# Optimization experiments

Measured on AMD Instinct MI355X. Metric: run time of the kernel, lower is better.

## Reference

```python
import jax, jax.numpy as jnp
import numpy as np

EPS = 1e-5

def _bn_relu(x, g, b, m, v):
    # inference batchnorm + relu, NCHW, fused affine
    scale = g * jax.lax.rsqrt(v + EPS)
    shift = b - m * scale
    return jnp.maximum(x * scale[None, :, None, None] + shift[None, :, None, None], 0.0)

def _conv1x1(x, w):
    # x: [B,C,H,W], w: [O,C]
    return jnp.einsum('bchw,oc->bohw', x, w)

def _xcorr_depthwise(search, kernel, padding=0):
    # search: [B,C,Hs,Ws], kernel: [B,C,Hk,Wk]; grouped conv, groups=B*C
    B, C, Hs, Ws = search.shape
    Hk, Wk = kernel.shape[2], kernel.shape[3]
    x = search.reshape(1, B * C, Hs, Ws)
    k = kernel.reshape(B * C, 1, Hk, Wk)
    out = jax.lax.conv_general_dilated(
        x, k, window_strides=(1, 1), padding=[(padding, padding), (padding, padding)],
        feature_group_count=B * C, dimension_numbers=('NCHW', 'OIHW', 'NCHW'))
    return out.reshape(B, C, out.shape[2], out.shape[3])

def setup_inputs():
    key = jax.random.key(0)
    ks = jax.random.split(key, 20)
    B, Cin, HID, COUT = 128, 256, 256, 20
    s = 1.0 / np.sqrt(Cin)
    inp = {
        'kernel': jax.random.normal(ks[0], (B, Cin, 7, 7), jnp.float32),
        'search': jax.random.normal(ks[1], (B, Cin, 31, 31), jnp.float32),
        # conv_kernel branch (1x1 conv weight stored as [O,C]) + BN stats
        'w_k': jax.random.normal(ks[2], (HID, Cin), jnp.float32) * s,
        'g_k': 1.0 + 0.1 * jax.random.normal(ks[3], (HID,), jnp.float32),
        'b_k': 0.1 * jax.random.normal(ks[4], (HID,), jnp.float32),
        'm_k': 0.1 * jax.random.normal(ks[5], (HID,), jnp.float32),
        'v_k': jax.random.uniform(ks[6], (HID,), jnp.float32, 0.5, 1.5),
        # conv_search branch
        'w_s': jax.random.normal(ks[7], (HID, Cin), jnp.float32) * s,
        'g_s': 1.0 + 0.1 * jax.random.normal(ks[8], (HID,), jnp.float32),
        'b_s': 0.1 * jax.random.normal(ks[9], (HID,), jnp.float32),
        'm_s': 0.1 * jax.random.normal(ks[10], (HID,), jnp.float32),
        'v_s': jax.random.uniform(ks[11], (HID,), jnp.float32, 0.5, 1.5),
        # head: conv1(1x1)+BN+ReLU, conv2(1x1, bias)
        'w_h1': jax.random.normal(ks[12], (HID, HID), jnp.float32) * (1.0 / np.sqrt(HID)),
        'g_h': 1.0 + 0.1 * jax.random.normal(ks[13], (HID,), jnp.float32),
        'b_h': 0.1 * jax.random.normal(ks[14], (HID,), jnp.float32),
        'm_h': 0.1 * jax.random.normal(ks[15], (HID,), jnp.float32),
        'v_h': jax.random.uniform(ks[16], (HID,), jnp.float32, 0.5, 1.5),
        'w_h2': jax.random.normal(ks[17], (COUT, HID), jnp.float32) * (1.0 / np.sqrt(HID)),
        'bias_h2': 0.1 * jax.random.normal(ks[18], (COUT,), jnp.float32),
    }
    return inp

def reference(kernel, search, w_k, g_k, b_k, m_k, v_k, w_s, g_s, b_s, m_s, v_s,
              w_h1, g_h, b_h, m_h, v_h, w_h2, bias_h2):
    k = _bn_relu(_conv1x1(kernel, w_k), g_k, b_k, m_k, v_k)   # [B,256,7,7]
    s = _bn_relu(_conv1x1(search, w_s), g_s, b_s, m_s, v_s)   # [B,256,31,31]
    feat = _xcorr_depthwise(s, k, padding=0)                  # [B,256,25,25]
    y = _bn_relu(_conv1x1(feat, w_h1), g_h, b_h, m_h, v_h)
    out = _conv1x1(y, w_h2) + bias_h2[None, :, None, None]    # [B,20,25,25]
    return out
```

## Files before the change

### kernel.cpp

```cpp
#include <hip/hip_runtime.h>
#include <hip/hip_fp16.h>

typedef _Float16 f16;
typedef __attribute__((ext_vector_type(8))) _Float16 f16x8;
typedef __attribute__((ext_vector_type(4))) _Float16 f16x4;
typedef __attribute__((ext_vector_type(2))) _Float16 f16x2;
typedef __attribute__((ext_vector_type(4))) float f32x4;

#define MFMA16(a, b, c) __builtin_amdgcn_mfma_f32_16x16x32_f16((a), (b), (c), 0, 0, 0)

#define OFF_WK   0u
#define OFF_WS   131072u
#define OFF_WH1  262144u
#define OFF_W2P  393216u
#define OFF_SH   409600u
#define OFF_S    412672u
#define OFF_KF   63392768u
#define OFF_FEAT 66604032u

__global__ __launch_bounds__(256) void prep_weights(
    const float* __restrict__ wk, const float* __restrict__ gk, const float* __restrict__ bk,
    const float* __restrict__ mk, const float* __restrict__ vk,
    const float* __restrict__ wsr, const float* __restrict__ gs, const float* __restrict__ bs,
    const float* __restrict__ ms, const float* __restrict__ vs,
    const float* __restrict__ wh1, const float* __restrict__ gh, const float* __restrict__ bh,
    const float* __restrict__ mh, const float* __restrict__ vh,
    const float* __restrict__ wh2,
    f16* __restrict__ wk16, f16* __restrict__ ws16, f16* __restrict__ wh116,
    f16* __restrict__ w2p, float* __restrict__ shifts) {
  int o = blockIdx.x;
  int t = threadIdx.x;
  float sck = gk[o] * rsqrtf(vk[o] + 1e-5f);
  float scs = gs[o] * rsqrtf(vs[o] + 1e-5f);
  float sch = gh[o] * rsqrtf(vh[o] + 1e-5f);
  int idx = o * 256 + t;
  wk16[idx]  = (f16)(wk[idx] * sck);
  ws16[idx]  = (f16)(wsr[idx] * scs);
  wh116[idx] = (f16)(wh1[idx] * sch);
  if (o < 32) w2p[idx] = (o < 20) ? (f16)wh2[idx] : (f16)0;
  if (t == 0) {
    shifts[o]       = bk[o] - mk[o] * sck;
    shifts[256 + o] = bs[o] - ms[o] * scs;
    shifts[512 + o] = bh[o] - mh[o] * sch;
  }
}

__device__ __forceinline__ int pi_row(int q, int r) {
  return (q ^ (r << 2)) + (r << 4);
}

template <int P>
__global__ __launch_bounds__(256) void conv_nchw(
    const float* __restrict__ X, const f16* __restrict__ W,
    const float* __restrict__ shift, f16* __restrict__ out) {
  const int C = 256;
  int n0 = blockIdx.x * 64;
  int t = threadIdx.x;
  int lane = t & 63, wave = t >> 6;
  int fm = lane & 15, kg = lane >> 4;

  __shared__ f16 Bs[2][64 * 40];

  int b0 = n0 / P, bp0 = n0 - b0 * P;
  bool safe = (bp0 + 64 <= P);

  int px = (t & 15) * 4;
  int cpr = (t >> 4) * 2;
  const float* xb = X + ((size_t)b0 * C) * P + bp0 + px;

  int ub[4], up[4];
  if (!safe) {
#pragma unroll
    for (int e = 0; e < 4; ++e) {
      int gn = n0 + px + e;
      ub[e] = gn / P;
      up[e] = gn - ub[e] * P;
    }
  }

  int wrow[4];
#pragma unroll
  for (int e = 0; e < 4; ++e) wrow[e] = pi_row(t & 15, e);
  int rrow[4];
#pragma unroll
  for (int nf = 0; nf < 4; ++nf) rrow[nf] = pi_row(nf * 4 + (fm >> 2), fm & 3);

  const f16* wp = W + (size_t)(wave * 64 + fm) * C + kg * 8;

  f32x4 rb[3][2];
#pragma unroll
  for (int s = 0; s < 3; ++s) {
    int cl = s * 32 + cpr;
    if (safe) {
      rb[s][0] = *(const f32x4*)(xb + (size_t)cl * P);
      rb[s][1] = *(const f32x4*)(xb + (size_t)(cl + 1) * P);
    } else {
#pragma unroll
      for (int e = 0; e < 4; ++e) {
        rb[s][0][e] = X[((size_t)ub[e] * C + cl) * P + up[e]];
        rb[s][1][e] = X[((size_t)ub[e] * C + cl + 1) * P + up[e]];
      }
    }
  }

  f32x4 acc[4][4] = {};
#pragma unroll
  for (int ci = 0; ci < 8; ++ci) {
    f16x8 a[4];
#pragma unroll
    for (int of = 0; of < 4; ++of)
      a[of] = *(const f16x8*)(wp + (size_t)of * 16 * C + ci * 32);

    f16* buf = Bs[ci & 1];
#pragma unroll
    for (int e = 0; e < 4; ++e) {
      f16x2 v;
      v[0] = (f16)rb[ci % 3][0][e];
      v[1] = (f16)rb[ci % 3][1][e];
      *(f16x2*)&buf[wrow[e] * 40 + cpr] = v;
    }
    if (ci + 3 < 8) {
      int cl = (ci + 3) * 32 + cpr;
      if (safe) {
        rb[ci % 3][0] = *(const f32x4*)(xb + (size_t)cl * P);
        rb[ci % 3][1] = *(const f32x4*)(xb + (size_t)(cl + 1) * P);
      } else {
#pragma unroll
        for (int e = 0; e < 4; ++e) {
          rb[ci % 3][0][e] = X[((size_t)ub[e] * C + cl) * P + up[e]];
          rb[ci % 3][1][e] = X[((size_t)ub[e] * C + cl + 1) * P + up[e]];
        }
      }
    }
    asm volatile("s_waitcnt lgkmcnt(0)" ::: "memory");
    __builtin_amdgcn_s_barrier();

    f16x8 b[4];
#pragma unroll
    for (int nf = 0; nf < 4; ++nf)
      b[nf] = *(const f16x8*)&buf[rrow[nf] * 40 + kg * 8];
#pragma unroll
    for (int of = 0; of < 4; ++of)
#pragma unroll
      for (int nf = 0; nf < 4; ++nf)
        acc[of][nf] = MFMA16(a[of], b[nf], acc[of][nf]);
  }

#pragma unroll
  for (int of = 0; of < 4; ++of) {
    int orow = wave * 64 + of * 16 + kg * 4;
    f32x4 sh = *(const f32x4*)(shift + orow);
#pragma unroll
    for (int nf = 0; nf < 4; ++nf) {
      int n = n0 + nf * 16 + fm;
      f16x4 st;
#pragma unroll
      for (int r = 0; r < 4; ++r)
        st[r] = (f16)fmaxf(acc[of][nf][r] + sh[r], 0.0f);
      *(f16x4*)(out + (size_t)n * C + orow) = st;
    }
  }
}

__global__ __launch_bounds__(256) void xcorr_dw_row(
    const f16* __restrict__ S ,
    const f16* __restrict__ K ,
    f16* __restrict__ F ) {
  int id = blockIdx.x;
  int x = id & 7;
  int r = id >> 3;
  int g = r % 7;
  int bq = r / 7;
  int b = bq * 8 + x;

  int wave = threadIdx.x >> 6;
  int lane = threadIdx.x & 63;
  int oi = g * 4 + wave;
  if (oi >= 25) return;

  const f16* Sb = S + (size_t)b * 961 * 256 + lane * 4;
  const f16* Kb = K + (size_t)b * 49 * 256 + lane * 4;

  f16x4 acc[25] = {};

  for (int di = 0; di < 7; ++di) {
    const f16* sp = Sb + (size_t)(oi + di) * 31 * 256;
    f16x4 srow[31];
#pragma unroll
    for (int j = 0; j < 31; ++j) srow[j] = *(const f16x4*)(sp + (size_t)j * 256);
    const f16* kp = Kb + (size_t)di * 7 * 256;
    f16x4 krow[7];
#pragma unroll
    for (int j = 0; j < 7; ++j) krow[j] = *(const f16x4*)(kp + (size_t)j * 256);

#pragma unroll
    for (int dj = 0; dj < 7; ++dj) {
      f16x4 kv = krow[dj];
#pragma unroll
      for (int oj = 0; oj < 25; ++oj)
        acc[oj] += srow[oj + dj] * kv;
    }
  }

  f16* Fb = F + ((size_t)b * 625 + (size_t)oi * 25) * 256 + lane * 4;
#pragma unroll
  for (int oj = 0; oj < 25; ++oj)
    *(f16x4*)(Fb + (size_t)oj * 256) = acc[oj];
}

__global__ __launch_bounds__(256) void head_fused(
    const f16* __restrict__ Xt ,
    const f16* __restrict__ W1, const float* __restrict__ shift,
    const f16* __restrict__ W2p , const float* __restrict__ bias,
    float* __restrict__ out ) {
  const int C = 256;
  int n0 = blockIdx.x * 64;
  int t = threadIdx.x;
  int lane = t & 63, wave = t >> 6;
  int fm = lane & 15, kg = lane >> 4;

  __shared__ f16 Ys[32][64][8];

  const f16* wp = W1 + (size_t)(wave * 64 + fm) * C + kg * 8;
  const f16* xp = Xt + (size_t)(n0 + fm) * C + kg * 8;

  f32x4 acc[4][4] = {};
#pragma unroll
  for (int c0 = 0; c0 < 256; c0 += 32) {
    f16x8 a[4], b[4];
#pragma unroll
    for (int of = 0; of < 4; ++of) a[of] = *(const f16x8*)(wp + (size_t)of * 16 * C + c0);
#pragma unroll
    for (int nf = 0; nf < 4; ++nf) b[nf] = *(const f16x8*)(xp + (size_t)nf * 16 * C + c0);
#pragma unroll
    for (int of = 0; of < 4; ++of)
#pragma unroll
      for (int nf = 0; nf < 4; ++nf)
        acc[of][nf] = MFMA16(a[of], b[nf], acc[of][nf]);
  }

#pragma unroll
  for (int of = 0; of < 4; ++of) {
    int orow = wave * 64 + of * 16 + kg * 4;
#pragma unroll
    for (int nf = 0; nf < 4; ++nf) {
      int n = nf * 16 + fm;
      f16x4 st;
#pragma unroll
      for (int r = 0; r < 4; ++r)
        st[r] = (f16)fmaxf(acc[of][nf][r] + shift[orow + r], 0.0f);
      *(f16x4*)&Ys[orow >> 3][n][(kg & 1) * 4] = st;
    }
  }
  __syncthreads();

  f32x4 acc2[2] = {};
#pragma unroll
  for (int c0 = 0; c0 < 256; c0 += 32) {
    f16x8 b = *(const f16x8*)&Ys[(c0 >> 3) + kg][wave * 16 + fm][0];
    f16x8 a0 = *(const f16x8*)(W2p + (size_t)fm * C + c0 + kg * 8);
    f16x8 a1 = *(const f16x8*)(W2p + (size_t)(16 + fm) * C + c0 + kg * 8);
    acc2[0] = MFMA16(a0, b, acc2[0]);
    acc2[1] = MFMA16(a1, b, acc2[1]);
  }

  int n = n0 + wave * 16 + fm;
  int bq = n / 625, bp = n - bq * 625;
  float* op = out + (size_t)bq * 12500 + bp;
#pragma unroll
  for (int of = 0; of < 2; ++of) {
#pragma unroll
    for (int r = 0; r < 4; ++r) {
      int o = of * 16 + kg * 4 + r;
      if (o < 20) op[(size_t)o * 625] = acc2[of][r] + bias[o];
    }
  }
}

extern "C" void kernel_launch(void* const* d_in, const int* in_sizes, int n_in,
                              void* d_out, int out_size, void* d_ws, size_t ws_size,
                              hipStream_t stream) {
  const float* kernel_in = (const float*)d_in[0];
  const float* search    = (const float*)d_in[1];
  const float* w_k = (const float*)d_in[2];
  const float* g_k = (const float*)d_in[3];
  const float* b_k = (const float*)d_in[4];
  const float* m_k = (const float*)d_in[5];
  const float* v_k = (const float*)d_in[6];
  const float* w_s = (const float*)d_in[7];
  const float* g_s = (const float*)d_in[8];
  const float* b_s = (const float*)d_in[9];
  const float* m_s = (const float*)d_in[10];
  const float* v_s = (const float*)d_in[11];
  const float* w_h1 = (const float*)d_in[12];
  const float* g_h = (const float*)d_in[13];
  const float* b_h = (const float*)d_in[14];
  const float* m_h = (const float*)d_in[15];
  const float* v_h = (const float*)d_in[16];
  const float* w_h2 = (const float*)d_in[17];
  const float* bias_h2 = (const float*)d_in[18];
  float* out = (float*)d_out;

  char* ws = (char*)d_ws;
  f16* wk16  = (f16*)(ws + OFF_WK);
  f16* ws16  = (f16*)(ws + OFF_WS);
  f16* wh116 = (f16*)(ws + OFF_WH1);
  f16* w2p   = (f16*)(ws + OFF_W2P);
  float* shifts = (float*)(ws + OFF_SH);
  f16* sbuf = (f16*)(ws + OFF_S);
  f16* kbuf = (f16*)(ws + OFF_KF);
  f16* fbuf = (f16*)(ws + OFF_FEAT);

  prep_weights<<<256, 256, 0, stream>>>(w_k, g_k, b_k, m_k, v_k,
                                        w_s, g_s, b_s, m_s, v_s,
                                        w_h1, g_h, b_h, m_h, v_h, w_h2,
                                        wk16, ws16, wh116, w2p, shifts);

  conv_nchw<961><<<dim3(1922), 256, 0, stream>>>(search, ws16, shifts + 256, sbuf);
  conv_nchw<49><<<dim3(98), 256, 0, stream>>>(kernel_in, wk16, shifts + 0, kbuf);

  xcorr_dw_row<<<dim3(896), 256, 0, stream>>>(sbuf, kbuf, fbuf);

  head_fused<<<dim3(1250), 256, 0, stream>>>(
      fbuf, wh116, shifts + 512, w2p, bias_h2, out);
}
```

Before: 172.5 us.

## Fuse depthwise xcorr with head convolutions via shared-memory feature tile

Merges the depthwise cross-correlation kernel and the two-layer 1x1 head into a single kernel. Each block computes up to 4 output rows (100 positions, padded to 112) of the xcorr result into an XOR-swizzled LDS tile, then runs both head GEMMs with MFMA directly from LDS. This removes the round trip of the 128x625x256 f16 feature map through global memory and one kernel launch. In exchange it uses 56KB of LDS per block, which may lower occupancy, wastes MFMA work on padded rows, and only reaches 896 blocks for the head stage.

```diff
diff --git a/kernel.cpp b/kernel.cpp
--- a/kernel.cpp
+++ b/kernel.cpp
@@ -16,7 +16,6 @@
 #define OFF_SH   409600u
 #define OFF_S    412672u
 #define OFF_KF   63392768u
-#define OFF_FEAT 66604032u
 
 __global__ __launch_bounds__(256) void prep_weights(
     const float* __restrict__ wk, const float* __restrict__ gk, const float* __restrict__ bk,
@@ -162,117 +161,136 @@
   }
 }
 
-__global__ __launch_bounds__(256) void xcorr_dw_row(
+__global__ __launch_bounds__(256) void xcorr_head(
     const f16* __restrict__ S ,
-    const f16* __restrict__ K ,
-    f16* __restrict__ F ) {
+    const f16* __restrict__ Kf ,
+    const f16* __restrict__ W1, const float* __restrict__ shift,
+    const f16* __restrict__ W2p, const float* __restrict__ bias,
+    float* __restrict__ out ) {
+  const int C = 256;
   int id = blockIdx.x;
   int x = id & 7;
   int r = id >> 3;
   int g = r % 7;
-  int bq = r / 7;
-  int b = bq * 8 + x;
-
-  int wave = threadIdx.x >> 6;
-  int lane = threadIdx.x & 63;
-  int oi = g * 4 + wave;
-  if (oi >= 25) return;
-
-  const f16* Sb = S + (size_t)b * 961 * 256 + lane * 4;
-  const f16* Kb = K + (size_t)b * 49 * 256 + lane * 4;
-
-  f16x4 acc[25] = {};
-
-  for (int di = 0; di < 7; ++di) {
-    const f16* sp = Sb + (size_t)(oi + di) * 31 * 256;
-    f16x4 srow[31];
-#pragma unroll
-    for (int j = 0; j < 31; ++j) srow[j] = *(const f16x4*)(sp + (size_t)j * 256);
-    const f16* kp = Kb + (size_t)di * 7 * 256;
-    f16x4 krow[7];
-#pragma unroll
-    for (int j = 0; j < 7; ++j) krow[j] = *(const f16x4*)(kp + (size_t)j * 256);
-
-#pragma unroll
-    for (int dj = 0; dj < 7; ++dj) {
-      f16x4 kv = krow[dj];
-#pragma unroll
-      for (int oj = 0; oj < 25; ++oj)
-        acc[oj] += srow[oj + dj] * kv;
-    }
-  }
-
-  f16* Fb = F + ((size_t)b * 625 + (size_t)oi * 25) * 256 + lane * 4;
-#pragma unroll
-  for (int oj = 0; oj < 25; ++oj)
-    *(f16x4*)(Fb + (size_t)oj * 256) = acc[oj];
-}
-
-__global__ __launch_bounds__(256) void head_fused(
-    const f16* __restrict__ Xt ,
-    const f16* __restrict__ W1, const float* __restrict__ shift,
-    const f16* __restrict__ W2p , const float* __restrict__ bias,
-    float* __restrict__ out ) {
-  const int C = 256;
-  int n0 = blockIdx.x * 64;
+  int b = (r / 7) * 8 + x;
+
   int t = threadIdx.x;
-  int lane = t & 63, wave = t >> 6;
+  int w = t >> 6, lane = t & 63;
   int fm = lane & 15, kg = lane >> 4;
-
-  __shared__ f16 Ys[32][64][8];
-
-  const f16* wp = W1 + (size_t)(wave * 64 + fm) * C + kg * 8;
-  const f16* xp = Xt + (size_t)(n0 + fm) * C + kg * 8;
-
-  f32x4 acc[4][4] = {};
-#pragma unroll
-  for (int c0 = 0; c0 < 256; c0 += 32) {
-    f16x8 a[4], b[4];
-#pragma unroll
-    for (int of = 0; of < 4; ++of) a[of] = *(const f16x8*)(wp + (size_t)of * 16 * C + c0);
-#pragma unroll
-    for (int nf = 0; nf < 4; ++nf) b[nf] = *(const f16x8*)(xp + (size_t)nf * 16 * C + c0);
+  int oi = g * 4 + w;
+
+  __shared__ char F[112 * 512];
+
+  if (oi < 25) {
+    const f16* Sb = S + (size_t)b * 961 * 256 + lane * 4;
+    const f16* Kb = Kf + (size_t)b * 49 * 256 + lane * 4;
+    f16x4 acc[25] = {};
+    for (int di = 0; di < 7; ++di) {
+      const f16* sp = Sb + (size_t)(oi + di) * 31 * 256;
+      f16x4 srow[31];
+#pragma unroll
+      for (int j = 0; j < 31; ++j) srow[j] = *(const f16x4*)(sp + (size_t)j * 256);
+      const f16* kp = Kb + (size_t)di * 7 * 256;
+      f16x4 krow[7];
+#pragma unroll
+      for (int j = 0; j < 7; ++j) krow[j] = *(const f16x4*)(kp + (size_t)j * 256);
+#pragma unroll
+      for (int dj = 0; dj < 7; ++dj) {
+        f16x4 kv = krow[dj];
+#pragma unroll
+        for (int oj = 0; oj < 25; ++oj)
+          acc[oj] += srow[oj + dj] * kv;
+      }
+    }
+#pragma unroll
+    for (int oj = 0; oj < 25; ++oj) {
+      int n = w * 25 + oj;
+      *(f16x4*)(F + ((n * 512 + lane * 8) ^ ((n & 7) << 4))) = acc[oj];
+    }
+  } else {
+    f16x4 z = {};
+#pragma unroll
+    for (int oj = 0; oj < 25; ++oj) {
+      int n = w * 25 + oj;
+      *(f16x4*)(F + ((n * 512 + lane * 8) ^ ((n & 7) << 4))) = z;
+    }
+  }
+  __syncthreads();
+
+  const f16* wp = W1 + (size_t)(w * 64 + fm) * C + kg * 8;
+  f32x4 acc1[4][7] = {};
+#pragma unroll
+  for (int ci = 0; ci < 8; ++ci) {
+    f16x8 a[4];
 #pragma unroll
     for (int of = 0; of < 4; ++of)
-#pragma unroll
-      for (int nf = 0; nf < 4; ++nf)
-        acc[of][nf] = MFMA16(a[of], b[nf], acc[of][nf]);
-  }
+      a[of] = *(const f16x8*)(wp + (size_t)of * 16 * C + ci * 32);
+    f16x8 bf[7];
+#pragma unroll
+    for (int nf = 0; nf < 7; ++nf) {
+      int n = nf * 16 + fm;
+      bf[nf] = *(const f16x8*)(F + ((n * 512 + (ci * 32 + kg * 8) * 2) ^ ((n & 7) << 4)));
+    }
+#pragma unroll
+    for (int of = 0; of < 4; ++of)
+#pragma unroll
+      for (int nf = 0; nf < 7; ++nf)
+        acc1[of][nf] = MFMA16(a[of], bf[nf], acc1[of][nf]);
+  }
+  __syncthreads();
 
 #pragma unroll
   for (int of = 0; of < 4; ++of) {
-    int orow = wave * 64 + of * 16 + kg * 4;
-#pragma unroll
-    for (int nf = 0; nf < 4; ++nf) {
+    int orow = w * 64 + of * 16 + kg * 4;
+    f32x4 sh = *(const f32x4*)(shift + orow);
+#pragma unroll
+    for (int nf = 0; nf < 7; ++nf) {
       int n = nf * 16 + fm;
       f16x4 st;
 #pragma unroll
-      for (int r = 0; r < 4; ++r)
-        st[r] = (f16)fmaxf(acc[of][nf][r] + shift[orow + r], 0.0f);
-      *(f16x4*)&Ys[orow >> 3][n][(kg & 1) * 4] = st;
+      for (int q = 0; q < 4; ++q)
+        st[q] = (f16)fmaxf(acc1[of][nf][q] + sh[q], 0.0f);
+      *(f16x4*)(F + ((n * 512 + orow * 2) ^ ((n & 7) << 4))) = st;
     }
   }
   __syncthreads();
 
-  f32x4 acc2[2] = {};
-#pragma unroll
-  for (int c0 = 0; c0 < 256; c0 += 32) {
-    f16x8 b = *(const f16x8*)&Ys[(c0 >> 3) + kg][wave * 16 + fm][0];
-    f16x8 a0 = *(const f16x8*)(W2p + (size_t)fm * C + c0 + kg * 8);
-    f16x8 a1 = *(const f16x8*)(W2p + (size_t)(16 + fm) * C + c0 + kg * 8);
-    acc2[0] = MFMA16(a0, b, acc2[0]);
-    acc2[1] = MFMA16(a1, b, acc2[1]);
-  }
-
-  int n = n0 + wave * 16 + fm;
-  int bq = n / 625, bp = n - bq * 625;
-  float* op = out + (size_t)bq * 12500 + bp;
-#pragma unroll
-  for (int of = 0; of < 2; ++of) {
-#pragma unroll
-    for (int r = 0; r < 4; ++r) {
-      int o = of * 16 + kg * 4 + r;
-      if (o < 20) op[(size_t)o * 625] = acc2[of][r] + bias[o];
+  f32x4 acc2[2][2] = {};
+  int nfa = w, nfb = w + 4;
+#pragma unroll
+  for (int ci = 0; ci < 8; ++ci) {
+    f16x8 a0 = *(const f16x8*)(W2p + (size_t)fm * C + ci * 32 + kg * 8);
+    f16x8 a1 = *(const f16x8*)(W2p + (size_t)(16 + fm) * C + ci * 32 + kg * 8);
+    int na = nfa * 16 + fm;
+    f16x8 b0 = *(const f16x8*)(F + ((na * 512 + (ci * 32 + kg * 8) * 2) ^ ((na & 7) << 4)));
+    acc2[0][0] = MFMA16(a0, b0, acc2[0][0]);
+    acc2[1][0] = MFMA16(a1, b0, acc2[1][0]);
+    if (nfb < 7) {
+      int nb = nfb * 16 + fm;
+      f16x8 b1 = *(const f16x8*)(F + ((nb * 512 + (ci * 32 + kg * 8) * 2) ^ ((nb & 7) << 4)));
+      acc2[0][1] = MFMA16(a0, b1, acc2[0][1]);
+      acc2[1][1] = MFMA16(a1, b1, acc2[1][1]);
+    }
+  }
+
+#pragma unroll
+  for (int q = 0; q < 2; ++q) {
+    int nf = q ? nfb : nfa;
+    if (nf >= 7) continue;
+    int n = nf * 16 + fm;
+    if (n < 100) {
+      int oi2 = g * 4 + n / 25;
+      int oj2 = n % 25;
+      if (oi2 < 25) {
+        float* op = out + (size_t)b * 12500 + oi2 * 25 + oj2;
+#pragma unroll
+        for (int of = 0; of < 2; ++of)
+#pragma unroll
+          for (int e = 0; e < 4; ++e) {
+            int o = of * 16 + kg * 4 + e;
+            if (o < 20) op[(size_t)o * 625] = acc2[of][q][e] + bias[o];
+          }
+      }
     }
   }
 }
@@ -309,7 +327,6 @@
   float* shifts = (float*)(ws + OFF_SH);
   f16* sbuf = (f16*)(ws + OFF_S);
   f16* kbuf = (f16*)(ws + OFF_KF);
-  f16* fbuf = (f16*)(ws + OFF_FEAT);
 
   prep_weights<<<256, 256, 0, stream>>>(w_k, g_k, b_k, m_k, v_k,
                                         w_s, g_s, b_s, m_s, v_s,
@@ -319,8 +336,6 @@
   conv_nchw<961><<<dim3(1922), 256, 0, stream>>>(search, ws16, shifts + 256, sbuf);
   conv_nchw<49><<<dim3(98), 256, 0, stream>>>(kernel_in, wk16, shifts + 0, kbuf);
 
-  xcorr_dw_row<<<dim3(896), 256, 0, stream>>>(sbuf, kbuf, fbuf);
-
-  head_fused<<<dim3(1250), 256, 0, stream>>>(
-      fbuf, wh116, shifts + 512, w2p, bias_h2, out);
-}
+  xcorr_head<<<dim3(896), 256, 0, stream>>>(
+      sbuf, kbuf, wh116, shifts + 512, w2p, bias_h2, out);
+}
```

Result: faster. 163.7 us (-5.1%).
